# Kernel optimization log

Hardware: AMD Instinct MI355X
Metric: run time of the kernel (lower is better)

Reference implementation:

```python
import jax, jax.numpy as jnp
import numpy as np

B, S, D = 32, 2048, 1024

def setup_inputs() -> dict:
    key = jax.random.key(0)
    k1, k2, k3 = jax.random.split(key, 3)
    embed_output = jax.random.normal(k1, (B, S, D), dtype=jnp.float32)
    mask = jax.random.randint(k2, (B, S), 0, 2) > 0  # bool [B,S]
    w = jax.random.normal(k3, (D, D), dtype=jnp.float32) * 0.05
    return {"embed_output": embed_output, "mask": mask, "w": w}

def reference(embed_output, mask, w):
    # ys: mean over sequence (NOTE: original does NOT mask the mean) -> [B,1,D]
    ys = jnp.mean(embed_output, axis=-2, keepdims=True)
    maskf = mask.astype(jnp.float32)
    # eW = (E @ W) * mask  -> [B,S,D]
    eW = jnp.einsum('bsd,de->bse', embed_output, w) * maskf[..., None]
    # f = dot(eW, ys) over last axis -> [B,S,1]
    f = jnp.sum(eW * ys, axis=-1, keepdims=True)
    # additive -1e9 bias where mask is False
    f = f + ((1.0 - maskf) * -1.0e9)[..., None]
    # softmax over sequence axis (-2)
    f = jax.nn.softmax(f, axis=-2)
    # weighted sum over sequence -> [B,D]
    zs = jnp.sum(f * embed_output, axis=-2)
    return zs, f
```

## Files before the change

### kernel.cpp

```cpp
#include <hip/hip_runtime.h>
#include <hip/hip_bf16.h>

#define B_ 32
#define S_ 2048
#define D_ 1024
#define NCH1 64
#define NCH3 128

__global__ __launch_bounds__(256) void k1_colsum(const float* __restrict__ E,
                                                 float* __restrict__ part_sums,
                                                 const unsigned int* __restrict__ mprobe,
                                                 int* __restrict__ flag) {
    int chunk = blockIdx.x, b = blockIdx.y, tid = threadIdx.x;
    if (chunk == 0 && b == 0 && tid < 64) {
        bool isI = true, isF = true;
        for (int i = tid * 4; i < tid * 4 + 4; ++i) {
            unsigned v = mprobe[i];
            if (v > 1u) isI = false;
            if (v != 0u && v != 0x3F800000u) isF = false;
        }
        unsigned long long bi = __ballot(isI);
        unsigned long long bf = __ballot(isF);
        if (tid == 0) {
            int f = 0;
            if (bi == ~0ull) f = 1;
            else if (bf == ~0ull) f = 2;
            *flag = f;
        }
    }
    const float4* base =
        (const float4*)(E + (size_t)(b * S_ + chunk * (S_ / NCH1)) * D_);
    float4 acc = make_float4(0.f, 0.f, 0.f, 0.f);
#pragma unroll 4
    for (int i = 0; i < S_ / NCH1; ++i) {
        float4 e = base[(size_t)i * (D_ / 4) + tid];
        acc.x += e.x; acc.y += e.y; acc.z += e.z; acc.w += e.w;
    }
    ((float4*)part_sums)[(size_t)(b * NCH1 + chunk) * (D_ / 4) + tid] = acc;
}

__global__ void k2a_ys(const float* __restrict__ part_sums, float* __restrict__ ys) {
    int g = blockIdx.x * 256 + threadIdx.x;
    int b = g >> 10, d = g & (D_ - 1);
    float s = 0.f;
#pragma unroll 8
    for (int k = 0; k < NCH1; ++k) s += part_sums[(size_t)(b * NCH1 + k) * D_ + d];
    ys[g] = s * (1.0f / S_);
}

__global__ __launch_bounds__(256) void k2b_v(const float* __restrict__ w,
                                             const float* __restrict__ ys,
                                             float* __restrict__ v) {
    int tid = threadIdx.x, wave = tid >> 6, lane = tid & 63;
    int d = blockIdx.x * 4 + wave;
    const float4* wrow = (const float4*)(w + (size_t)d * D_);
    float4 w0 = wrow[lane], w1 = wrow[64 + lane], w2 = wrow[128 + lane], w3 = wrow[192 + lane];
    for (int b = 0; b < B_; ++b) {
        const float4* yb = (const float4*)(ys + (size_t)b * D_);
        float4 y0 = yb[lane], y1 = yb[64 + lane], y2 = yb[128 + lane], y3 = yb[192 + lane];
        float p = w0.x * y0.x + w0.y * y0.y + w0.z * y0.z + w0.w * y0.w;
        p += w1.x * y1.x + w1.y * y1.y + w1.z * y1.z + w1.w * y1.w;
        p += w2.x * y2.x + w2.y * y2.y + w2.z * y2.z + w2.w * y2.w;
        p += w3.x * y3.x + w3.y * y3.y + w3.z * y3.z + w3.w * y3.w;
#pragma unroll
        for (int off = 32; off; off >>= 1) p += __shfl_xor(p, off, 64);
        if (lane == 0) v[(size_t)b * D_ + d] = p;
    }
}

__global__ __launch_bounds__(256) void k3_fused(
    const float* __restrict__ E, const void* __restrict__ maskp,
    const float* __restrict__ v, const int* __restrict__ flagp,
    float* __restrict__ logits, float* __restrict__ part_l,
    float* __restrict__ part_z) {
    int chunk = (NCH3 - 1) - blockIdx.x, b = (B_ - 1) - blockIdx.y;
    int tid = threadIdx.x, wave = tid >> 6, lane = tid & 63;
    int mf = *flagp;
    const int* mi = (const int*)maskp;
    const unsigned char* mu = (const unsigned char*)maskp;
    const float* mfl = (const float*)maskp;

    const float4* vf = (const float4*)(v + (size_t)b * D_);
    float4 v0 = vf[lane], v1 = vf[64 + lane], v2 = vf[128 + lane], v3 = vf[192 + lane];

    int s0 = chunk * 16 + wave * 4;
    const float4* row0 = (const float4*)(E + (size_t)(b * S_ + s0) * D_);

    float4 e[4][4];
#pragma unroll
    for (int i = 0; i < 4; ++i) {
        const float4* row = row0 + (size_t)i * (D_ / 4);
        e[i][0] = row[lane]; e[i][1] = row[64 + lane];
        e[i][2] = row[128 + lane]; e[i][3] = row[192 + lane];
    }
    float lg4[4], wt4[4];
#pragma unroll
    for (int i = 0; i < 4; ++i) {
        float p = e[i][0].x * v0.x + e[i][0].y * v0.y + e[i][0].z * v0.z + e[i][0].w * v0.w;
        p += e[i][1].x * v1.x + e[i][1].y * v1.y + e[i][1].z * v1.z + e[i][1].w * v1.w;
        p += e[i][2].x * v2.x + e[i][2].y * v2.y + e[i][2].z * v2.z + e[i][2].w * v2.w;
        p += e[i][3].x * v3.x + e[i][3].y * v3.y + e[i][3].z * v3.z + e[i][3].w * v3.w;
#pragma unroll
        for (int off = 32; off; off >>= 1) p += __shfl_xor(p, off, 64);
        int idx = b * S_ + s0 + i;
        int mv = (mf == 1) ? (mi[idx] != 0)
                           : (mf == 2 ? (mfl[idx] != 0.0f) : (mu[idx] != 0));
        lg4[i] = mv ? p : -1.0e9f;
        wt4[i] = mv ? __expf(p) : 0.0f;
    }
    if (lane == 0)
        *(float4*)(logits + (size_t)b * S_ + s0) =
            make_float4(lg4[0], lg4[1], lg4[2], lg4[3]);

    float4 z0 = make_float4(0.f, 0.f, 0.f, 0.f), z1 = z0, z2 = z0, z3 = z0;
#pragma unroll
    for (int i = 0; i < 4; ++i) {
        float pe = wt4[i];
        z0.x += pe * e[i][0].x; z0.y += pe * e[i][0].y; z0.z += pe * e[i][0].z; z0.w += pe * e[i][0].w;
        z1.x += pe * e[i][1].x; z1.y += pe * e[i][1].y; z1.z += pe * e[i][1].z; z1.w += pe * e[i][1].w;
        z2.x += pe * e[i][2].x; z2.y += pe * e[i][2].y; z2.z += pe * e[i][2].z; z2.w += pe * e[i][2].w;
        z3.x += pe * e[i][3].x; z3.y += pe * e[i][3].y; z3.z += pe * e[i][3].z; z3.w += pe * e[i][3].w;
    }

    __shared__ float4 zbuf[4][256];
    __shared__ float lw[4];
    zbuf[wave][lane] = z0; zbuf[wave][64 + lane] = z1;
    zbuf[wave][128 + lane] = z2; zbuf[wave][192 + lane] = z3;
    if (lane == 0) lw[wave] = wt4[0] + wt4[1] + wt4[2] + wt4[3];
    __syncthreads();
    float4 a0 = zbuf[0][tid], a1 = zbuf[1][tid], a2 = zbuf[2][tid], a3 = zbuf[3][tid];
    float4 r = make_float4(a0.x + a1.x + a2.x + a3.x, a0.y + a1.y + a2.y + a3.y,
                           a0.z + a1.z + a2.z + a3.z, a0.w + a1.w + a2.w + a3.w);
    ((float4*)(part_z + (size_t)(b * NCH3 + chunk) * D_))[tid] = r;
    if (tid == 0) part_l[b * NCH3 + chunk] = lw[0] + lw[1] + lw[2] + lw[3];
}

__global__ __launch_bounds__(256) void k4_merge_f(
    const float* __restrict__ part_l, const float* __restrict__ part_z,
    const float* __restrict__ logits, float* __restrict__ out_zs,
    float* __restrict__ out_f) {
    int b = blockIdx.x, tid = threadIdx.x;
    __shared__ float pl_s[NCH3];
    if (tid < NCH3) pl_s[tid] = part_l[b * NCH3 + tid];
    __syncthreads();
    float lsum = 0.f;
#pragma unroll 8
    for (int i = 0; i < NCH3; ++i) lsum += pl_s[i];
    float4 acc = make_float4(0.f, 0.f, 0.f, 0.f);
    for (int i = 0; i < NCH3; ++i) {
        float4 zv = ((const float4*)(part_z + (size_t)(b * NCH3 + i) * D_))[tid];
        acc.x += zv.x; acc.y += zv.y; acc.z += zv.z; acc.w += zv.w;
    }
    float inv = 1.0f / lsum;
    ((float4*)(out_zs + (size_t)b * D_))[tid] =
        make_float4(acc.x * inv, acc.y * inv, acc.z * inv, acc.w * inv);
    const float4* lrow = (const float4*)(logits + (size_t)b * S_);
    float4* frow = (float4*)(out_f + (size_t)b * S_);
#pragma unroll
    for (int j = 0; j < 2; ++j) {
        float4 lv = lrow[j * 256 + tid];
        frow[j * 256 + tid] = make_float4(__expf(lv.x) * inv, __expf(lv.y) * inv,
                                          __expf(lv.z) * inv, __expf(lv.w) * inv);
    }
}

extern "C" void kernel_launch(void* const* d_in, const int* in_sizes, int n_in,
                              void* d_out, int out_size, void* d_ws, size_t ws_size,
                              hipStream_t stream) {
    const float* E = (const float*)d_in[0];
    const void* maskp = d_in[1];
    const float* w = (const float*)d_in[2];
    float* out = (float*)d_out;

    float* ws = (float*)d_ws;
    float* part_sums = ws;
    float* ys = part_sums + (size_t)B_ * NCH1 * D_;
    float* v = ys + (size_t)B_ * D_;
    float* logits = v + (size_t)B_ * D_;
    float* part_l = logits + (size_t)B_ * S_;
    float* part_z = part_l + B_ * NCH3;
    int* flag = (int*)(part_z + (size_t)B_ * NCH3 * D_);

    k1_colsum<<<dim3(NCH1, B_), 256, 0, stream>>>(E, part_sums,
                                                  (const unsigned int*)maskp, flag);
    k2a_ys<<<(B_ * D_) / 256, 256, 0, stream>>>(part_sums, ys);
    k2b_v<<<D_ / 4, 256, 0, stream>>>(w, ys, v);
    k3_fused<<<dim3(NCH3, B_), 256, 0, stream>>>(E, maskp, v, flag, logits,
                                                 part_l, part_z);
    k4_merge_f<<<B_, 256, 0, stream>>>(part_l, part_z, logits,
                                       out, out + B_ * D_);
}
```

Measured before the change: 442.2 us.

## Emit per-wave partials in attention pass and parallelize merge across D slices

```diff
diff --git a/kernel.cpp b/kernel.cpp
--- a/kernel.cpp
+++ b/kernel.cpp
@@ -4,8 +4,8 @@
 #define B_ 32
 #define S_ 2048
 #define D_ 1024
-#define NCH1 64
-#define NCH3 128
+#define NCH1 32
+#define NW3 256
 
 __global__ __launch_bounds__(256) void k1_colsum(const float* __restrict__ E,
                                                  float* __restrict__ part_sums,
@@ -73,8 +73,9 @@
     const float* __restrict__ v, const int* __restrict__ flagp,
     float* __restrict__ logits, float* __restrict__ part_l,
     float* __restrict__ part_z) {
-    int chunk = (NCH3 - 1) - blockIdx.x, b = (B_ - 1) - blockIdx.y;
+    int b = blockIdx.y;
     int tid = threadIdx.x, wave = tid >> 6, lane = tid & 63;
+    int c = blockIdx.x * 4 + wave;
     int mf = *flagp;
     const int* mi = (const int*)maskp;
     const unsigned char* mu = (const unsigned char*)maskp;
@@ -83,84 +84,94 @@
     const float4* vf = (const float4*)(v + (size_t)b * D_);
     float4 v0 = vf[lane], v1 = vf[64 + lane], v2 = vf[128 + lane], v3 = vf[192 + lane];
 
-    int s0 = chunk * 16 + wave * 4;
-    const float4* row0 = (const float4*)(E + (size_t)(b * S_ + s0) * D_);
-
-    float4 e[4][4];
-#pragma unroll
-    for (int i = 0; i < 4; ++i) {
-        const float4* row = row0 + (size_t)i * (D_ / 4);
-        e[i][0] = row[lane]; e[i][1] = row[64 + lane];
-        e[i][2] = row[128 + lane]; e[i][3] = row[192 + lane];
-    }
-    float lg4[4], wt4[4];
-#pragma unroll
-    for (int i = 0; i < 4; ++i) {
-        float p = e[i][0].x * v0.x + e[i][0].y * v0.y + e[i][0].z * v0.z + e[i][0].w * v0.w;
-        p += e[i][1].x * v1.x + e[i][1].y * v1.y + e[i][1].z * v1.z + e[i][1].w * v1.w;
-        p += e[i][2].x * v2.x + e[i][2].y * v2.y + e[i][2].z * v2.z + e[i][2].w * v2.w;
-        p += e[i][3].x * v3.x + e[i][3].y * v3.y + e[i][3].z * v3.z + e[i][3].w * v3.w;
-#pragma unroll
-        for (int off = 32; off; off >>= 1) p += __shfl_xor(p, off, 64);
-        int idx = b * S_ + s0 + i;
-        int mv = (mf == 1) ? (mi[idx] != 0)
-                           : (mf == 2 ? (mfl[idx] != 0.0f) : (mu[idx] != 0));
-        lg4[i] = mv ? p : -1.0e9f;
-        wt4[i] = mv ? __expf(p) : 0.0f;
-    }
-    if (lane == 0)
-        *(float4*)(logits + (size_t)b * S_ + s0) =
-            make_float4(lg4[0], lg4[1], lg4[2], lg4[3]);
-
     float4 z0 = make_float4(0.f, 0.f, 0.f, 0.f), z1 = z0, z2 = z0, z3 = z0;
-#pragma unroll
-    for (int i = 0; i < 4; ++i) {
-        float pe = wt4[i];
-        z0.x += pe * e[i][0].x; z0.y += pe * e[i][0].y; z0.z += pe * e[i][0].z; z0.w += pe * e[i][0].w;
-        z1.x += pe * e[i][1].x; z1.y += pe * e[i][1].y; z1.z += pe * e[i][1].z; z1.w += pe * e[i][1].w;
-        z2.x += pe * e[i][2].x; z2.y += pe * e[i][2].y; z2.z += pe * e[i][2].z; z2.w += pe * e[i][2].w;
-        z3.x += pe * e[i][3].x; z3.y += pe * e[i][3].y; z3.z += pe * e[i][3].z; z3.w += pe * e[i][3].w;
-    }
-
-    __shared__ float4 zbuf[4][256];
-    __shared__ float lw[4];
-    zbuf[wave][lane] = z0; zbuf[wave][64 + lane] = z1;
-    zbuf[wave][128 + lane] = z2; zbuf[wave][192 + lane] = z3;
-    if (lane == 0) lw[wave] = wt4[0] + wt4[1] + wt4[2] + wt4[3];
-    __syncthreads();
-    float4 a0 = zbuf[0][tid], a1 = zbuf[1][tid], a2 = zbuf[2][tid], a3 = zbuf[3][tid];
-    float4 r = make_float4(a0.x + a1.x + a2.x + a3.x, a0.y + a1.y + a2.y + a3.y,
-                           a0.z + a1.z + a2.z + a3.z, a0.w + a1.w + a2.w + a3.w);
-    ((float4*)(part_z + (size_t)(b * NCH3 + chunk) * D_))[tid] = r;
-    if (tid == 0) part_l[b * NCH3 + chunk] = lw[0] + lw[1] + lw[2] + lw[3];
+    float lacc = 0.f;
+
+#pragma unroll
+    for (int g = 0; g < 2; ++g) {
+        int s0 = c * 8 + g * 4;
+        const float4* row0 = (const float4*)(E + (size_t)(b * S_ + s0) * D_);
+        float4 e[4][4];
+#pragma unroll
+        for (int i = 0; i < 4; ++i) {
+            const float4* row = row0 + (size_t)i * (D_ / 4);
+            e[i][0] = row[lane]; e[i][1] = row[64 + lane];
+            e[i][2] = row[128 + lane]; e[i][3] = row[192 + lane];
+        }
+        float lg4[4], wt4[4];
+#pragma unroll
+        for (int i = 0; i < 4; ++i) {
+            float p = e[i][0].x * v0.x + e[i][0].y * v0.y + e[i][0].z * v0.z + e[i][0].w * v0.w;
+            p += e[i][1].x * v1.x + e[i][1].y * v1.y + e[i][1].z * v1.z + e[i][1].w * v1.w;
+            p += e[i][2].x * v2.x + e[i][2].y * v2.y + e[i][2].z * v2.z + e[i][2].w * v2.w;
+            p += e[i][3].x * v3.x + e[i][3].y * v3.y + e[i][3].z * v3.z + e[i][3].w * v3.w;
+#pragma unroll
+            for (int off = 32; off; off >>= 1) p += __shfl_xor(p, off, 64);
+            int idx = b * S_ + s0 + i;
+            int mv = (mf == 1) ? (mi[idx] != 0)
+                               : (mf == 2 ? (mfl[idx] != 0.0f) : (mu[idx] != 0));
+            lg4[i] = mv ? p : -1.0e9f;
+            wt4[i] = mv ? __expf(p) : 0.0f;
+        }
+        if (lane == 0)
+            *(float4*)(logits + (size_t)b * S_ + s0) =
+                make_float4(lg4[0], lg4[1], lg4[2], lg4[3]);
+#pragma unroll
+        for (int i = 0; i < 4; ++i) {
+            float pe = wt4[i];
+            z0.x += pe * e[i][0].x; z0.y += pe * e[i][0].y; z0.z += pe * e[i][0].z; z0.w += pe * e[i][0].w;
+            z1.x += pe * e[i][1].x; z1.y += pe * e[i][1].y; z1.z += pe * e[i][1].z; z1.w += pe * e[i][1].w;
+            z2.x += pe * e[i][2].x; z2.y += pe * e[i][2].y; z2.z += pe * e[i][2].z; z2.w += pe * e[i][2].w;
+            z3.x += pe * e[i][3].x; z3.y += pe * e[i][3].y; z3.z += pe * e[i][3].z; z3.w += pe * e[i][3].w;
+        }
+        lacc += wt4[0] + wt4[1] + wt4[2] + wt4[3];
+    }
+
+    float4* pz = (float4*)(part_z + (size_t)(b * NW3 + c) * D_);
+    pz[lane] = z0; pz[64 + lane] = z1; pz[128 + lane] = z2; pz[192 + lane] = z3;
+    if (lane == 0) part_l[b * NW3 + c] = lacc;
 }
 
 __global__ __launch_bounds__(256) void k4_merge_f(
     const float* __restrict__ part_l, const float* __restrict__ part_z,
     const float* __restrict__ logits, float* __restrict__ out_zs,
     float* __restrict__ out_f) {
-    int b = blockIdx.x, tid = threadIdx.x;
-    __shared__ float pl_s[NCH3];
-    if (tid < NCH3) pl_s[tid] = part_l[b * NCH3 + tid];
+    int x = blockIdx.x, b = blockIdx.y, tid = threadIdx.x;
+    int cg = tid >> 5, d4 = tid & 31;
+    __shared__ float pl_s[NW3];
+    __shared__ float4 red[8][32];
+
+    float4 acc = make_float4(0.f, 0.f, 0.f, 0.f);
+#pragma unroll 4
+    for (int k = 0; k < NW3 / 8; ++k) {
+        int c = cg + k * 8;
+        float4 zv = ((const float4*)part_z)[(size_t)(b * NW3 + c) * (D_ / 4) + x * 32 + d4];
+        acc.x += zv.x; acc.y += zv.y; acc.z += zv.z; acc.w += zv.w;
+    }
+    red[cg][d4] = acc;
+    pl_s[tid] = part_l[b * NW3 + tid];
     __syncthreads();
+
     float lsum = 0.f;
 #pragma unroll 8
-    for (int i = 0; i < NCH3; ++i) lsum += pl_s[i];
-    float4 acc = make_float4(0.f, 0.f, 0.f, 0.f);
-    for (int i = 0; i < NCH3; ++i) {
-        float4 zv = ((const float4*)(part_z + (size_t)(b * NCH3 + i) * D_))[tid];
-        acc.x += zv.x; acc.y += zv.y; acc.z += zv.z; acc.w += zv.w;
-    }
+    for (int i = 0; i < NW3; ++i) lsum += pl_s[i];
     float inv = 1.0f / lsum;
-    ((float4*)(out_zs + (size_t)b * D_))[tid] =
-        make_float4(acc.x * inv, acc.y * inv, acc.z * inv, acc.w * inv);
-    const float4* lrow = (const float4*)(logits + (size_t)b * S_);
-    float4* frow = (float4*)(out_f + (size_t)b * S_);
-#pragma unroll
-    for (int j = 0; j < 2; ++j) {
-        float4 lv = lrow[j * 256 + tid];
-        frow[j * 256 + tid] = make_float4(__expf(lv.x) * inv, __expf(lv.y) * inv,
-                                          __expf(lv.z) * inv, __expf(lv.w) * inv);
+
+    if (tid < 32) {
+        float4 t = red[0][tid];
+#pragma unroll
+        for (int j = 1; j < 8; ++j) {
+            float4 u = red[j][tid];
+            t.x += u.x; t.y += u.y; t.z += u.z; t.w += u.w;
+        }
+        ((float4*)out_zs)[b * (D_ / 4) + x * 32 + tid] =
+            make_float4(t.x * inv, t.y * inv, t.z * inv, t.w * inv);
+    }
+    if (tid < 64) {
+        float4 lv = ((const float4*)logits)[b * (S_ / 4) + x * 64 + tid];
+        ((float4*)out_f)[b * (S_ / 4) + x * 64 + tid] =
+            make_float4(__expf(lv.x) * inv, __expf(lv.y) * inv,
+                        __expf(lv.z) * inv, __expf(lv.w) * inv);
     }
 }
 
@@ -178,15 +189,15 @@
     float* v = ys + (size_t)B_ * D_;
     float* logits = v + (size_t)B_ * D_;
     float* part_l = logits + (size_t)B_ * S_;
-    float* part_z = part_l + B_ * NCH3;
-    int* flag = (int*)(part_z + (size_t)B_ * NCH3 * D_);
+    float* part_z = part_l + B_ * NW3;
+    int* flag = (int*)(part_z + (size_t)B_ * NW3 * D_);
 
     k1_colsum<<<dim3(NCH1, B_), 256, 0, stream>>>(E, part_sums,
                                                   (const unsigned int*)maskp, flag);
     k2a_ys<<<(B_ * D_) / 256, 256, 0, stream>>>(part_sums, ys);
     k2b_v<<<D_ / 4, 256, 0, stream>>>(w, ys, v);
-    k3_fused<<<dim3(NCH3, B_), 256, 0, stream>>>(E, maskp, v, flag, logits,
-                                                 part_l, part_z);
-    k4_merge_f<<<B_, 256, 0, stream>>>(part_l, part_z, logits,
-                                       out, out + B_ * D_);
-}
+    k3_fused<<<dim3(NW3 / 4, B_), 256, 0, stream>>>(E, maskp, v, flag, logits,
+                                                    part_l, part_z);
+    k4_merge_f<<<dim3(8, B_), 256, 0, stream>>>(part_l, part_z, logits,
+                                                out, out + B_ * D_);
+}
```

New measurement: 438.2 us. Within noise of the previous version (-0.9%).
